# Kernel tuning notes

Measured on AMD Instinct MI355X. Metric: run time of the kernel, lower is better.

Reference implementation:

```python
import jax, jax.numpy as jnp
import numpy as np

B, IN_C, OUT_C, K, Z_DIM = 32, 128, 128, 3, 512
H, W, STRIDE = 56, 56, 1


def setup_inputs() -> dict:
    key = jax.random.key(0)
    k1, k2, k3 = jax.random.split(key, 3)
    x = jax.random.normal(k1, (B, IN_C, H, W), dtype=jnp.float32)
    z = jax.random.normal(k2, (B, Z_DIM), dtype=jnp.float32)
    # nn.Linear(z_dim, out_c*in_c*k*k): weight [out_f, in_f], bias [out_f]
    out_f = OUT_C * IN_C * K * K
    W_head = jax.random.normal(k3, (out_f, Z_DIM), dtype=jnp.float32) * (1.0 / np.sqrt(Z_DIM))
    b_head = jnp.zeros((out_f,), dtype=jnp.float32)
    return {"x": x, "z": z, "W_head": W_head, "b_head": b_head}


def reference(x, z, W_head, b_head):
    b = x.shape[0]
    # hypernetwork head: per-sample conv weights
    w = z @ W_head.T + b_head                       # [B, out_c*in_c*k*k]
    w = w.reshape(b, OUT_C, IN_C, K, K)             # [B, O, I, K, K]

    pad = K // 2

    def conv_one(xi, wi):
        # xi: [I, H, W], wi: [O, I, K, K] -> [O, H', W']
        out = jax.lax.conv_general_dilated(
            xi[None],                                # [1, I, H, W]
            wi,
            window_strides=(STRIDE, STRIDE),
            padding=[(pad, pad), (pad, pad)],
            dimension_numbers=("NCHW", "OIHW", "NCHW"),
        )
        return out[0]

    return jax.vmap(conv_one)(x, w)                 # [B, O, H', W']
```

## Files before the change

kernel.cpp:

```cpp
#include <hip/hip_runtime.h>
#include <hip/hip_bf16.h>
#include <stdint.h>

#define BB 32
#define IC 128
#define OC 128
#define HH 56
#define WW 56
#define ZD 512
#define NRS 9
#define OI (OC*IC)
#define WROWS (OI*NRS)
#define WDIM 58
#define NHEADBLK (WROWS / 64)
#define NTRBLK (HH * BB)
#define XTILE (4 * WDIM * 256)

typedef float  f32x4  __attribute__((ext_vector_type(4)));
typedef short  bf16x8 __attribute__((ext_vector_type(8)));

static __device__ __forceinline__ short f2bf(float f) {
    uint32_t u = __float_as_uint(f);
    uint32_t r = (u + 0x7fffu + ((u >> 16) & 1u)) >> 16;
    return (short)r;
}
static __device__ __forceinline__ short f2bf_hw(float f) {
    __hip_bfloat16 h = __float2bfloat16(f);
    return *reinterpret_cast<short*>(&h);
}
static __device__ __forceinline__ float bf2f(short s) {
    uint32_t u = ((uint32_t)(uint16_t)s) << 16;
    return __uint_as_float(u);
}
static __device__ __forceinline__ void gll16(const void* g, void* l) {
    __builtin_amdgcn_global_load_lds(
        (const __attribute__((address_space(1))) uint32_t*)g,
        (__attribute__((address_space(3))) uint32_t*)l, 16, 0, 0);
}

__global__ __launch_bounds__(256, 2) void fused_head_tr_kernel(
    const float* __restrict__ Wh, const float* __restrict__ z,
    short* __restrict__ wnat,
    const float* __restrict__ x, short* __restrict__ xt)
{
    if (blockIdx.x >= NHEADBLK) {
        const int bx = blockIdx.x - NHEADBLK;
        const int b = bx / HH;
        const int h = bx - b * HH;
        const int w = threadIdx.x & 63;
        const int yq = threadIdx.x >> 6;
        if (w >= WW) return;
        const float* xp = x + (size_t)b * IC * HH * WW + h * WW + w;
        short* op = xt + (((size_t)(b * HH + h)) * WW + w) * IC;
        #pragma unroll
        for (int q = 0; q < 4; ++q) {
            int ic = yq * 4 + q;
            bf16x8 pk;
            #pragma unroll
            for (int j = 0; j < 8; ++j) {
                float v = xp[(size_t)(ic * 8 + j) * (HH * WW)];
                pk[j] = f2bf(v);
            }
            *(bf16x8*)(op + ic * 8) = pk;
        }
        return;
    }

    __shared__ __align__(16) char Zl[32 * 1024];
    const int tid  = threadIdx.x;
    const int lane = tid & 63;
    const int wv   = tid >> 6;

    {
        const int b = tid >> 3, ks = (tid & 7) * 64;
        const float* zp = z + (size_t)b * ZD + ks;
        const int bx = (b & 7) << 4;
        #pragma unroll
        for (int j8 = 0; j8 < 8; ++j8) {
            f32x4 v0 = *(const f32x4*)(zp + j8 * 8);
            f32x4 v1 = *(const f32x4*)(zp + j8 * 8 + 4);
            bf16x8 pk;
            pk[0] = f2bf_hw(v0.x); pk[1] = f2bf_hw(v0.y);
            pk[2] = f2bf_hw(v0.z); pk[3] = f2bf_hw(v0.w);
            pk[4] = f2bf_hw(v1.x); pk[5] = f2bf_hw(v1.y);
            pk[6] = f2bf_hw(v1.z); pk[7] = f2bf_hw(v1.w);
            *(bf16x8*)(Zl + b * 1024 + ((ks * 2 + j8 * 16) ^ bx)) = pk;
        }
    }
    __syncthreads();

    const int rl = lane & 15;
    const int kq = lane >> 4;
    const int zxor = (rl & 7) << 4;
    const int rowg = blockIdx.x * 64 + wv * 16 + rl;

    const char* wp = (const char*)Wh + (size_t)rowg * (ZD * 4) + kq * 32;

    f32x4 wd[32];
    #pragma unroll
    for (int i = 0; i < 16; ++i) {
        wd[2 * i]     = *(const f32x4*)(wp + i * 128);
        wd[2 * i + 1] = *(const f32x4*)(wp + i * 128 + 16);
    }

    f32x4 acc0 = {0.f, 0.f, 0.f, 0.f}, acc1 = {0.f, 0.f, 0.f, 0.f};
    #pragma unroll
    for (int kb = 0; kb < 16; ++kb) {
        const int koff = (kb * 64 + kq * 16) ^ zxor;
        bf16x8 a0 = *(const bf16x8*)(Zl + rl * 1024 + koff);
        bf16x8 a1 = *(const bf16x8*)(Zl + (16 + rl) * 1024 + koff);
        f32x4 lo = wd[2 * kb];
        f32x4 hi = wd[2 * kb + 1];
        bf16x8 bw;
        bw[0] = f2bf_hw(lo.x); bw[1] = f2bf_hw(lo.y);
        bw[2] = f2bf_hw(lo.z); bw[3] = f2bf_hw(lo.w);
        bw[4] = f2bf_hw(hi.x); bw[5] = f2bf_hw(hi.y);
        bw[6] = f2bf_hw(hi.z); bw[7] = f2bf_hw(hi.w);
        acc0 = __builtin_amdgcn_mfma_f32_16x16x32_bf16(a0, bw, acc0, 0, 0, 0);
        acc1 = __builtin_amdgcn_mfma_f32_16x16x32_bf16(a1, bw, acc1, 0, 0, 0);
    }

    #pragma unroll
    for (int reg = 0; reg < 4; ++reg) {
        const int b0 = kq * 4 + reg;
        wnat[(size_t)b0 * WROWS + rowg]        = f2bf(acc0[reg]);
        wnat[(size_t)(16 + b0) * WROWS + rowg] = f2bf(acc1[reg]);
    }
}

__global__ __launch_bounds__(256) void repack_kernel(
    const short* __restrict__ wnat, const float* __restrict__ bh,
    short* __restrict__ wbf)
{
    const int b = blockIdx.y;
    const int oi0 = blockIdx.x * 2048 + threadIdx.x * 8;
    const short* src = wnat + (size_t)b * WROWS + (size_t)oi0 * 9;
    const float* bp  = bh + (size_t)oi0 * 9;

    bf16x8 in[9];
    #pragma unroll
    for (int j = 0; j < 9; ++j) in[j] = *(const bf16x8*)(src + j * 8);
    f32x4 bv[18];
    #pragma unroll
    for (int m = 0; m < 18; ++m) bv[m] = *(const f32x4*)(bp + m * 4);

    #pragma unroll
    for (int rs = 0; rs < 9; ++rs) {
        bf16x8 o;
        #pragma unroll
        for (int jj = 0; jj < 8; ++jj) {
            const int e = jj * 9 + rs;
            float v = bf2f(in[e >> 3][e & 7]) + bv[e >> 2][e & 3];
            o[jj] = f2bf(v);
        }
        *(bf16x8*)(wbf + ((size_t)(b * 9 + rs)) * OI + oi0) = o;
    }
}

__global__ __launch_bounds__(512) void conv_kernel(
    const short* __restrict__ wbf,
    const short* __restrict__ xt,
    float* __restrict__ out)
{
    __shared__ __align__(16) char Xl[XTILE];
    __shared__ __align__(16) char Wl[3][32768];
    const int tid  = threadIdx.x;
    const int lane = tid & 63;
    const int wv   = tid >> 6;
    const int og   = wv & 3;
    const int hh   = wv >> 2;
    const int h0 = blockIdx.x * 2;
    const int b  = blockIdx.y;

    #pragma unroll
    for (int q = 0; q < 8; ++q) {
        int idx = tid + q * 512;
        if (idx < XTILE / 16) ((f32x4*)Xl)[idx] = (f32x4){0.f, 0.f, 0.f, 0.f};
    }
    __syncthreads();

    for (int r = 0; r < 4; ++r) {
        int hin = h0 + r - 1;
        if (hin < 0 || hin >= HH) continue;
        const char* src = (const char*)(xt + ((size_t)(b * HH + hin)) * WW * IC);
        char* dstb = Xl + (r * WDIM + 1) * 256;
        for (int it = wv; it < 14; it += 8) {
            int c = it * 64 + lane;
            int u = r * WDIM + 1 + (c >> 4);
            int soff = (c * 16) ^ ((u & 7) << 4);
            gll16(src + soff, dstb + it * 1024);
        }
    }

    #define STAGE_CW(rs_, buf_)                                                 \
        {                                                                       \
            const char* ws_ = (const char*)(wbf +                               \
                ((size_t)b * NRS + (rs_)) * OI);                                \
            _Pragma("unroll")                                                   \
            for (int it_ = 0; it_ < 4; ++it_) {                                 \
                int c_ = (wv * 4 + it_) * 64 + lane;                            \
                int so_ = (c_ * 16) ^ (((c_ >> 4) & 7) << 4);                   \
                gll16(ws_ + so_, Wl[buf_] + (wv * 4 + it_) * 1024);             \
            }                                                                   \
        }

    STAGE_CW(0, 0);

    f32x4 acc[2][4];
    #pragma unroll
    for (int a = 0; a < 2; ++a)
        #pragma unroll
        for (int p = 0; p < 4; ++p) acc[a][p] = (f32x4){0.f, 0.f, 0.f, 0.f};

    const int axor = (lane & 7) << 4;
    int kkoff[4];
    #pragma unroll
    for (int kk = 0; kk < 4; ++kk) kkoff[kk] = kk * 64 + ((lane >> 4) << 4);

    for (int rs = 0; rs < 9; ++rs) {
        if (rs < 8) STAGE_CW(rs + 1, (rs + 1) % 3);
        if (rs == 8) { asm volatile("s_waitcnt vmcnt(0)" ::: "memory"); }
        else         { asm volatile("s_waitcnt vmcnt(4)" ::: "memory"); }
        __builtin_amdgcn_sched_barrier(0);
        __builtin_amdgcn_s_barrier();
        __builtin_amdgcn_sched_barrier(0);

        const char* Wb = Wl[rs % 3];
        const int r = rs / 3, s = rs - 3 * r;
        int ubase[4], bswz[4];
        #pragma unroll
        for (int pf = 0; pf < 4; ++pf) {
            int p = pf * 16 + (lane & 15);
            int pc = p > 55 ? 55 : p;
            int uu = (hh + r) * WDIM + pc + s;
            ubase[pf] = uu * 256;
            bswz[pf] = (uu & 7) << 4;
        }
        #pragma unroll
        for (int kk = 0; kk < 4; ++kk) {
            bf16x8 a0 = *(const bf16x8*)(Wb + (og * 32 + (lane & 15)) * 256 +
                                         (kkoff[kk] ^ axor));
            bf16x8 a1 = *(const bf16x8*)(Wb + (og * 32 + 16 + (lane & 15)) * 256 +
                                         (kkoff[kk] ^ axor));
            #pragma unroll
            for (int pf = 0; pf < 4; ++pf) {
                bf16x8 bv = *(const bf16x8*)(Xl + ubase[pf] + (kkoff[kk] ^ bswz[pf]));
                acc[0][pf] = __builtin_amdgcn_mfma_f32_16x16x32_bf16(a0, bv, acc[0][pf], 0, 0, 0);
                acc[1][pf] = __builtin_amdgcn_mfma_f32_16x16x32_bf16(a1, bv, acc[1][pf], 0, 0, 0);
            }
        }
    }
    #undef STAGE_CW

    const int pcol = lane & 15;
    const int rowq = lane >> 4;
    const int hO = h0 + hh;
    #pragma unroll
    for (int aa = 0; aa < 2; ++aa) {
        int o0 = og * 32 + aa * 16 + rowq * 4;
        #pragma unroll
        for (int pf = 0; pf < 4; ++pf) {
            int p = pf * 16 + pcol;
            if (p < WW) {
                #pragma unroll
                for (int reg = 0; reg < 4; ++reg) {
                    out[(((size_t)b * OC + (o0 + reg)) * HH + hO) * WW + p] = acc[aa][pf][reg];
                }
            }
        }
    }
}

extern "C" void kernel_launch(void* const* d_in, const int* in_sizes, int n_in,
                              void* d_out, int out_size, void* d_ws, size_t ws_size,
                              hipStream_t stream) {
    const float* x  = (const float*)d_in[0];
    const float* z  = (const float*)d_in[1];
    const float* Wh = (const float*)d_in[2];
    const float* bh = (const float*)d_in[3];
    float* out = (float*)d_out;

    short* wnat = (short*)d_ws;
    short* wbf  = (short*)((char*)d_ws + 9437184);
    short* xt   = (short*)((char*)d_ws + 18874368);

    fused_head_tr_kernel<<<dim3(NHEADBLK + NTRBLK), 256, 0, stream>>>(Wh, z, wnat, x, xt);
    repack_kernel<<<dim3(8, 32), 256, 0, stream>>>(wnat, bh, wbf);
    conv_kernel<<<dim3(HH / 2, BB), 512, 0, stream>>>(wbf, xt, out);
}
```

Measured before the change: 158.1 us.

## Fuse weight repack into head GEMM and widen conv per-wave output tile

The hypernetwork head kernel now uses 576-thread blocks covering 144 weight rows (16 oi × 9 taps). It adds the bias and transposes the result through shared memory, writing the conv-ready bf16 layout directly. This removes the separate repack kernel and the intermediate wnat round trip through global memory. The head's register loading of W is split into two halves with prefetch to reduce register pressure. Separately, the conv kernel drops to 256 threads, with each wave computing 64 output channels instead of 32, which raises A-fragment reuse at the cost of more accumulators per thread.

Result: faster. 153.8 us (-2.7%).

```diff
diff --git a/kernel.cpp b/kernel.cpp
--- a/kernel.cpp
+++ b/kernel.cpp
@@ -12,12 +12,13 @@
 #define OI (OC*IC)
 #define WROWS (OI*NRS)
 #define WDIM 58
-#define NHEADBLK (WROWS / 64)
+#define NHEADBLK 1024
 #define NTRBLK (HH * BB)
 #define XTILE (4 * WDIM * 256)
 
 typedef float  f32x4  __attribute__((ext_vector_type(4)));
 typedef short  bf16x8 __attribute__((ext_vector_type(8)));
+typedef short  s16x4  __attribute__((ext_vector_type(4)));
 
 static __device__ __forceinline__ short f2bf(float f) {
     uint32_t u = __float_as_uint(f);
@@ -38,23 +39,25 @@
         (__attribute__((address_space(3))) uint32_t*)l, 16, 0, 0);
 }
 
-__global__ __launch_bounds__(256, 2) void fused_head_tr_kernel(
+__global__ __launch_bounds__(576, 1) void fused_head_tr_kernel(
     const float* __restrict__ Wh, const float* __restrict__ z,
-    short* __restrict__ wnat,
+    const float* __restrict__ bh, short* __restrict__ wbf,
     const float* __restrict__ x, short* __restrict__ xt)
 {
     if (blockIdx.x >= NHEADBLK) {
         const int bx = blockIdx.x - NHEADBLK;
         const int b = bx / HH;
         const int h = bx - b * HH;
-        const int w = threadIdx.x & 63;
-        const int yq = threadIdx.x >> 6;
+        const int tid = threadIdx.x;
+        if (tid >= 512) return;
+        const int w = tid & 63;
+        const int yq = tid >> 6;
         if (w >= WW) return;
         const float* xp = x + (size_t)b * IC * HH * WW + h * WW + w;
         short* op = xt + (((size_t)(b * HH + h)) * WW + w) * IC;
         #pragma unroll
-        for (int q = 0; q < 4; ++q) {
-            int ic = yq * 4 + q;
+        for (int q = 0; q < 2; ++q) {
+            int ic = yq * 2 + q;
             bf16x8 pk;
             #pragma unroll
             for (int j = 0; j < 8; ++j) {
@@ -67,11 +70,12 @@
     }
 
     __shared__ __align__(16) char Zl[32 * 1024];
+    __shared__ __align__(16) char Sl[144 * 64];
     const int tid  = threadIdx.x;
     const int lane = tid & 63;
     const int wv   = tid >> 6;
 
-    {
+    if (tid < 256) {
         const int b = tid >> 3, ks = (tid & 7) * 64;
         const float* zp = z + (size_t)b * ZD + ks;
         const int bx = (b & 7) << 4;
@@ -92,13 +96,14 @@
     const int rl = lane & 15;
     const int kq = lane >> 4;
     const int zxor = (rl & 7) << 4;
-    const int rowg = blockIdx.x * 64 + wv * 16 + rl;
+    const int rowLocal = wv * 16 + rl;
+    const int rowg = blockIdx.x * 144 + rowLocal;
 
     const char* wp = (const char*)Wh + (size_t)rowg * (ZD * 4) + kq * 32;
 
-    f32x4 wd[32];
-    #pragma unroll
-    for (int i = 0; i < 16; ++i) {
+    f32x4 wd[16];
+    #pragma unroll
+    for (int i = 0; i < 8; ++i) {
         wd[2 * i]     = *(const f32x4*)(wp + i * 128);
         wd[2 * i + 1] = *(const f32x4*)(wp + i * 128 + 16);
     }
@@ -106,11 +111,12 @@
     f32x4 acc0 = {0.f, 0.f, 0.f, 0.f}, acc1 = {0.f, 0.f, 0.f, 0.f};
     #pragma unroll
     for (int kb = 0; kb < 16; ++kb) {
+        const int sl = kb & 7;
         const int koff = (kb * 64 + kq * 16) ^ zxor;
         bf16x8 a0 = *(const bf16x8*)(Zl + rl * 1024 + koff);
         bf16x8 a1 = *(const bf16x8*)(Zl + (16 + rl) * 1024 + koff);
-        f32x4 lo = wd[2 * kb];
-        f32x4 hi = wd[2 * kb + 1];
+        f32x4 lo = wd[2 * sl];
+        f32x4 hi = wd[2 * sl + 1];
         bf16x8 bw;
         bw[0] = f2bf_hw(lo.x); bw[1] = f2bf_hw(lo.y);
         bw[2] = f2bf_hw(lo.z); bw[3] = f2bf_hw(lo.w);
@@ -118,46 +124,41 @@
         bw[6] = f2bf_hw(hi.z); bw[7] = f2bf_hw(hi.w);
         acc0 = __builtin_amdgcn_mfma_f32_16x16x32_bf16(a0, bw, acc0, 0, 0, 0);
         acc1 = __builtin_amdgcn_mfma_f32_16x16x32_bf16(a1, bw, acc1, 0, 0, 0);
-    }
-
-    #pragma unroll
-    for (int reg = 0; reg < 4; ++reg) {
-        const int b0 = kq * 4 + reg;
-        wnat[(size_t)b0 * WROWS + rowg]        = f2bf(acc0[reg]);
-        wnat[(size_t)(16 + b0) * WROWS + rowg] = f2bf(acc1[reg]);
-    }
-}
-
-__global__ __launch_bounds__(256) void repack_kernel(
-    const short* __restrict__ wnat, const float* __restrict__ bh,
-    short* __restrict__ wbf)
-{
-    const int b = blockIdx.y;
-    const int oi0 = blockIdx.x * 2048 + threadIdx.x * 8;
-    const short* src = wnat + (size_t)b * WROWS + (size_t)oi0 * 9;
-    const float* bp  = bh + (size_t)oi0 * 9;
-
-    bf16x8 in[9];
-    #pragma unroll
-    for (int j = 0; j < 9; ++j) in[j] = *(const bf16x8*)(src + j * 8);
-    f32x4 bv[18];
-    #pragma unroll
-    for (int m = 0; m < 18; ++m) bv[m] = *(const f32x4*)(bp + m * 4);
-
-    #pragma unroll
-    for (int rs = 0; rs < 9; ++rs) {
-        bf16x8 o;
-        #pragma unroll
-        for (int jj = 0; jj < 8; ++jj) {
-            const int e = jj * 9 + rs;
-            float v = bf2f(in[e >> 3][e & 7]) + bv[e >> 2][e & 3];
-            o[jj] = f2bf(v);
-        }
-        *(bf16x8*)(wbf + ((size_t)(b * 9 + rs)) * OI + oi0) = o;
-    }
-}
-
-__global__ __launch_bounds__(512) void conv_kernel(
+        if (kb < 8) {
+            wd[2 * sl]     = *(const f32x4*)(wp + (kb + 8) * 128);
+            wd[2 * sl + 1] = *(const f32x4*)(wp + (kb + 8) * 128 + 16);
+        }
+    }
+
+    {
+        const int swz = (rowLocal & 7) << 3;
+        s16x4 s0, s1;
+        #pragma unroll
+        for (int reg = 0; reg < 4; ++reg) {
+            s0[reg] = f2bf(acc0[reg]);
+            s1[reg] = f2bf(acc1[reg]);
+        }
+        *(s16x4*)(Sl + rowLocal * 64 + ((kq * 8) ^ swz))      = s0;
+        *(s16x4*)(Sl + rowLocal * 64 + ((32 + kq * 8) ^ swz)) = s1;
+    }
+    __syncthreads();
+
+    if (tid < 512) {
+        const int b  = tid >> 4;
+        const int oiL = tid & 15;
+        const int oi = blockIdx.x * 16 + oiL;
+        #pragma unroll
+        for (int rs = 0; rs < 9; ++rs) {
+            const int rowL = oiL * 9 + rs;
+            short sh = *(const short*)(Sl + rowL * 64 +
+                                       ((2 * b) ^ ((rowL & 7) << 3)));
+            float v = bf2f(sh) + bh[(size_t)oi * 9 + rs];
+            wbf[((size_t)(b * 9 + rs)) * OI + oi] = f2bf(v);
+        }
+    }
+}
+
+__global__ __launch_bounds__(256) void conv_kernel(
     const short* __restrict__ wbf,
     const short* __restrict__ xt,
     float* __restrict__ out)
@@ -167,14 +168,14 @@
     const int tid  = threadIdx.x;
     const int lane = tid & 63;
     const int wv   = tid >> 6;
-    const int og   = wv & 3;
-    const int hh   = wv >> 2;
+    const int og   = wv & 1;
+    const int hh   = wv >> 1;
     const int h0 = blockIdx.x * 2;
     const int b  = blockIdx.y;
 
     #pragma unroll
-    for (int q = 0; q < 8; ++q) {
-        int idx = tid + q * 512;
+    for (int q = 0; q < 15; ++q) {
+        int idx = tid + q * 256;
         if (idx < XTILE / 16) ((f32x4*)Xl)[idx] = (f32x4){0.f, 0.f, 0.f, 0.f};
     }
     __syncthreads();
@@ -184,7 +185,7 @@
         if (hin < 0 || hin >= HH) continue;
         const char* src = (const char*)(xt + ((size_t)(b * HH + hin)) * WW * IC);
         char* dstb = Xl + (r * WDIM + 1) * 256;
-        for (int it = wv; it < 14; it += 8) {
+        for (int it = wv; it < 14; it += 4) {
             int c = it * 64 + lane;
             int u = r * WDIM + 1 + (c >> 4);
             int soff = (c * 16) ^ ((u & 7) << 4);
@@ -197,18 +198,18 @@
             const char* ws_ = (const char*)(wbf +                               \
                 ((size_t)b * NRS + (rs_)) * OI);                                \
             _Pragma("unroll")                                                   \
-            for (int it_ = 0; it_ < 4; ++it_) {                                 \
-                int c_ = (wv * 4 + it_) * 64 + lane;                            \
+            for (int it_ = 0; it_ < 8; ++it_) {                                 \
+                int c_ = (wv * 8 + it_) * 64 + lane;                            \
                 int so_ = (c_ * 16) ^ (((c_ >> 4) & 7) << 4);                   \
-                gll16(ws_ + so_, Wl[buf_] + (wv * 4 + it_) * 1024);             \
+                gll16(ws_ + so_, Wl[buf_] + (wv * 8 + it_) * 1024);             \
             }                                                                   \
         }
 
     STAGE_CW(0, 0);
 
-    f32x4 acc[2][4];
-    #pragma unroll
-    for (int a = 0; a < 2; ++a)
+    f32x4 acc[4][4];
+    #pragma unroll
+    for (int a = 0; a < 4; ++a)
         #pragma unroll
         for (int p = 0; p < 4; ++p) acc[a][p] = (f32x4){0.f, 0.f, 0.f, 0.f};
 
@@ -220,7 +221,7 @@
     for (int rs = 0; rs < 9; ++rs) {
         if (rs < 8) STAGE_CW(rs + 1, (rs + 1) % 3);
         if (rs == 8) { asm volatile("s_waitcnt vmcnt(0)" ::: "memory"); }
-        else         { asm volatile("s_waitcnt vmcnt(4)" ::: "memory"); }
+        else         { asm volatile("s_waitcnt vmcnt(8)" ::: "memory"); }
         __builtin_amdgcn_sched_barrier(0);
         __builtin_amdgcn_s_barrier();
         __builtin_amdgcn_sched_barrier(0);
@@ -238,15 +239,18 @@
         }
         #pragma unroll
         for (int kk = 0; kk < 4; ++kk) {
-            bf16x8 a0 = *(const bf16x8*)(Wb + (og * 32 + (lane & 15)) * 256 +
-                                         (kkoff[kk] ^ axor));
-            bf16x8 a1 = *(const bf16x8*)(Wb + (og * 32 + 16 + (lane & 15)) * 256 +
-                                         (kkoff[kk] ^ axor));
+            bf16x8 av[4];
+            #pragma unroll
+            for (int af = 0; af < 4; ++af)
+                av[af] = *(const bf16x8*)(Wb + (og * 64 + af * 16 + (lane & 15)) * 256 +
+                                          (kkoff[kk] ^ axor));
             #pragma unroll
             for (int pf = 0; pf < 4; ++pf) {
                 bf16x8 bv = *(const bf16x8*)(Xl + ubase[pf] + (kkoff[kk] ^ bswz[pf]));
-                acc[0][pf] = __builtin_amdgcn_mfma_f32_16x16x32_bf16(a0, bv, acc[0][pf], 0, 0, 0);
-                acc[1][pf] = __builtin_amdgcn_mfma_f32_16x16x32_bf16(a1, bv, acc[1][pf], 0, 0, 0);
+                #pragma unroll
+                for (int af = 0; af < 4; ++af)
+                    acc[af][pf] = __builtin_amdgcn_mfma_f32_16x16x32_bf16(
+                        av[af], bv, acc[af][pf], 0, 0, 0);
             }
         }
     }
@@ -256,15 +260,15 @@
     const int rowq = lane >> 4;
     const int hO = h0 + hh;
     #pragma unroll
-    for (int aa = 0; aa < 2; ++aa) {
-        int o0 = og * 32 + aa * 16 + rowq * 4;
+    for (int af = 0; af < 4; ++af) {
+        int o0 = og * 64 + af * 16 + rowq * 4;
         #pragma unroll
         for (int pf = 0; pf < 4; ++pf) {
             int p = pf * 16 + pcol;
             if (p < WW) {
                 #pragma unroll
                 for (int reg = 0; reg < 4; ++reg) {
-                    out[(((size_t)b * OC + (o0 + reg)) * HH + hO) * WW + p] = acc[aa][pf][reg];
+                    out[(((size_t)b * OC + (o0 + reg)) * HH + hO) * WW + p] = acc[af][pf][reg];
                 }
             }
         }
@@ -280,11 +284,9 @@
     const float* bh = (const float*)d_in[3];
     float* out = (float*)d_out;
 
-    short* wnat = (short*)d_ws;
-    short* wbf  = (short*)((char*)d_ws + 9437184);
-    short* xt   = (short*)((char*)d_ws + 18874368);
-
-    fused_head_tr_kernel<<<dim3(NHEADBLK + NTRBLK), 256, 0, stream>>>(Wh, z, wnat, x, xt);
-    repack_kernel<<<dim3(8, 32), 256, 0, stream>>>(wnat, bh, wbf);
-    conv_kernel<<<dim3(HH / 2, BB), 512, 0, stream>>>(wbf, xt, out);
-}
+    short* wbf = (short*)d_ws;
+    short* xt  = (short*)((char*)d_ws + 9437184);
+
+    fused_head_tr_kernel<<<dim3(NHEADBLK + NTRBLK), 576, 0, stream>>>(Wh, z, bh, wbf, x, xt);
+    conv_kernel<<<dim3(HH / 2, BB), 256, 0, stream>>>(wbf, xt, out);
+}
```
